# Kernel optimization log

Hardware: AMD Instinct MI355X
Metric: run time of the kernel (lower is better)

Reference implementation:

```python
import jax, jax.numpy as jnp
import numpy as np

S, D = 4096, 2048  # seq_len, embedding_space == qkv_dim


def setup_inputs() -> dict:
    key = jax.random.key(0)
    k1, k2, k3, k4, k5 = jax.random.split(key, 5)
    return {
        "input_embedding": jax.random.normal(k1, (S, D), dtype=jnp.float32),
        "query_embedding": jax.random.normal(k2, (S, D), dtype=jnp.float32),
        "Wq": jax.random.normal(k3, (D, D), dtype=jnp.float32) * 0.02,
        "Wk": jax.random.normal(k4, (D, D), dtype=jnp.float32) * 0.02,
        "Wv": jax.random.normal(k5, (D, D), dtype=jnp.float32) * 0.02,
        "include_mask": 0,  # False -> causal mask applied (module's inverted logic)
    }


def reference(input_embedding, query_embedding, Wq, Wk, Wv, include_mask):
    q = query_embedding @ Wq          # [S, D]
    k = input_embedding @ Wk          # [S, D]
    v = input_embedding @ Wv          # [S, D]
    scores = (q @ k.T) / 10.0         # [S, S]; module hardcodes /10, not sqrt(d)
    if not include_mask:
        # causal: -inf strictly above the diagonal (triu with offset 1)
        s = scores.shape[0]
        causal = jnp.tril(jnp.ones((s, s), dtype=bool))
        scores = jnp.where(causal, scores, -jnp.inf)
    probs = jax.nn.softmax(scores, axis=-1)
    return probs @ v                  # [S, D]
```

## Files before the change

### kernel.cpp

```cpp
#include <hip/hip_runtime.h>
#include <hip/hip_bf16.h>
#include <math.h>

typedef __bf16 bf16_t;
typedef __bf16 bf16x8 __attribute__((ext_vector_type(8)));
typedef float f32x4 __attribute__((ext_vector_type(4)));

enum { EP_BF16 = 0, EP_SCORES = 1, EP_F32 = 2 };

__device__ __forceinline__ void gload_lds16(const void* g, void* l) {
  __builtin_amdgcn_global_load_lds(
      (const __attribute__((address_space(1))) void*)g,
      (__attribute__((address_space(3))) void*)l, 16, 0, 0);
}

__device__ __forceinline__ int xcd_swz(int bid, int nwg) {
  const int q = nwg >> 3;
  return (bid & 7) * q + (bid >> 3);
}


template <int TM, bool STG>
__device__ __forceinline__ void do_tile(char* smem, int slot, int sslot, size_t stoff,
                                        const char* const* gbase, const int* lbase,
                                        const int* aoff, const int* boff,
                                        f32x4 (&acc)[TM][4]) {
  bf16x8 bfr[4], af[4];
  if constexpr (TM == 8) {
    if constexpr (STG) {
      gload_lds16(gbase[0] + stoff, smem + sslot + lbase[0]);
      gload_lds16(gbase[1] + stoff, smem + sslot + lbase[1]);
    }
#pragma unroll
    for (int n = 0; n < 4; ++n) bfr[n] = *(const bf16x8*)(smem + slot + boff[n]);
#pragma unroll
    for (int m = 0; m < 4; ++m) af[m] = *(const bf16x8*)(smem + slot + aoff[m]);
    __builtin_amdgcn_s_setprio(1);
#pragma unroll
    for (int m = 0; m < 4; ++m)
#pragma unroll
      for (int n = 0; n < 4; ++n)
        acc[m][n] = __builtin_amdgcn_mfma_f32_16x16x32_bf16(af[m], bfr[n], acc[m][n], 0, 0, 0);
    __builtin_amdgcn_s_setprio(0);
    if constexpr (STG) __builtin_amdgcn_s_barrier();
    if constexpr (STG) {
      gload_lds16(gbase[2] + stoff, smem + sslot + lbase[2]);
      gload_lds16(gbase[3] + stoff, smem + sslot + lbase[3]);
    }
#pragma unroll
    for (int m = 0; m < 4; ++m) af[m] = *(const bf16x8*)(smem + slot + aoff[4 + m]);
    __builtin_amdgcn_s_setprio(1);
#pragma unroll
    for (int m = 0; m < 4; ++m)
#pragma unroll
      for (int n = 0; n < 4; ++n)
        acc[4 + m][n] = __builtin_amdgcn_mfma_f32_16x16x32_bf16(af[m], bfr[n], acc[4 + m][n], 0, 0, 0);
    __builtin_amdgcn_s_setprio(0);
  } else {
    if constexpr (STG) {
      gload_lds16(gbase[0] + stoff, smem + sslot + lbase[0]);
      gload_lds16(gbase[1] + stoff, smem + sslot + lbase[1]);
      gload_lds16(gbase[2] + stoff, smem + sslot + lbase[2]);
    }
#pragma unroll
    for (int n = 0; n < 4; ++n) bfr[n] = *(const bf16x8*)(smem + slot + boff[n]);
#pragma unroll
    for (int m = 0; m < 4; ++m) af[m] = *(const bf16x8*)(smem + slot + aoff[m]);
    __builtin_amdgcn_s_setprio(1);
#pragma unroll
    for (int m = 0; m < 4; ++m)
#pragma unroll
      for (int n = 0; n < 4; ++n)
        acc[m][n] = __builtin_amdgcn_mfma_f32_16x16x32_bf16(af[m], bfr[n], acc[m][n], 0, 0, 0);
    __builtin_amdgcn_s_setprio(0);
  }
}

template <int TM, int EPI>
__device__ __forceinline__ void gemm_core(
    const bf16_t* __restrict__ A, const bf16_t* __restrict__ B,
    void* __restrict__ Cout, int M, int N, int K,
    int row0, int col0, bool causal, float scale, char* smem)
{
  constexpr int BM = TM * 32;
  constexpr int LPT_A = BM / 128;
  constexpr int LPT = LPT_A + 2;
  constexpr int ABYTES = BM * 64;
  constexpr int SLOT = (BM + 256) * 64;

  const int tid = threadIdx.x;
  const int w = tid >> 6, lane = tid & 63;
  const int wr = w >> 2, wc = w & 3;

  int Keff = K;
  if (EPI == EP_F32 && causal) Keff = min(K, row0 + BM);
  const int nt = Keff >> 5;

  const char* gbase[LPT];
  int lbase[LPT];
  {
    const int sd = (tid & 3) ^ ((tid >> 3) & 3);
    const int rrow = tid >> 2;
#pragma unroll
    for (int r = 0; r < LPT; ++r) {
      const bool isA = (r < LPT_A);
      const int rr = isA ? r : (r - LPT_A);
      const int R = rr * 128 + rrow;
      const int grow = (isA ? row0 : col0) + R;
      const bf16_t* op = isA ? A : B;
      gbase[r] = (const char*)(op + (size_t)grow * K) + sd * 16;
      lbase[r] = (isA ? 0 : ABYTES) + rr * 8192 + w * 1024;
    }
  }

  const int fl = lane & 15;
  const int arow_off = fl * 64 + (((lane >> 4) ^ ((fl >> 1) & 3)) * 16);
  int aoff[TM], boff[4];
#pragma unroll
  for (int m = 0; m < TM; ++m) aoff[m] = (wr * (TM * 16) + m * 16) * 64 + arow_off;
#pragma unroll
  for (int n = 0; n < 4; ++n) boff[n] = ABYTES + (wc * 64 + n * 16) * 64 + arow_off;

  f32x4 acc[TM][4] = {};

  const int npro = nt < 3 ? nt : 3;
  for (int t = 0; t < npro; ++t)
#pragma unroll
    for (int r = 0; r < LPT; ++r)
      gload_lds16(gbase[r] + (size_t)t * 64, smem + (t & 3) * SLOT + lbase[r]);

  const int nmain = nt - 3;
  for (int t = 0; t < nmain; ++t) {
    if constexpr (TM == 8) asm volatile("s_waitcnt vmcnt(8)" ::: "memory");
    else                   asm volatile("s_waitcnt vmcnt(6)" ::: "memory");
    __builtin_amdgcn_s_barrier();
    asm volatile("" ::: "memory");
    __builtin_amdgcn_sched_barrier(0);
    do_tile<TM, true>(smem, (t & 3) * SLOT, ((t + 3) & 3) * SLOT,
                      (size_t)(t + 3) * 64, gbase, lbase, aoff, boff, acc);
  }

  asm volatile("s_waitcnt vmcnt(0)" ::: "memory");
  __builtin_amdgcn_s_barrier();
  asm volatile("" ::: "memory");
  __builtin_amdgcn_sched_barrier(0);
  for (int t = nmain > 0 ? nmain : 0; t < nt; ++t)
    do_tile<TM, false>(smem, (t & 3) * SLOT, 0, 0, gbase, lbase, aoff, boff, acc);

  const int cr = (lane >> 4) * 4;
  const int cc = lane & 15;
#pragma unroll
  for (int m = 0; m < TM; ++m) {
#pragma unroll
    for (int n = 0; n < 4; ++n) {
#pragma unroll
      for (int i = 0; i < 4; ++i) {
        const int r = row0 + wr * (TM * 16) + m * 16 + cr + i;
        const int c = col0 + wc * 64 + n * 16 + cc;
        float v = acc[m][n][i];
        if (EPI == EP_BF16) {
          ((bf16_t*)Cout)[(size_t)r * N + c] = (bf16_t)v;
        } else if (EPI == EP_SCORES) {
          v *= scale;
          if (causal && c > r) v = -INFINITY;
          ((float*)Cout)[(size_t)r * N + c] = v;
        } else {
          ((float*)Cout)[(size_t)r * N + c] = v;
        }
      }
    }
  }
}

__launch_bounds__(512, 2)
__global__ void qk_k(const bf16_t* __restrict__ qe16, const bf16_t* __restrict__ ie16,
                     const bf16_t* __restrict__ WqT, const bf16_t* __restrict__ WkT,
                     bf16_t* __restrict__ q16, bf16_t* __restrict__ k16) {
  extern __shared__ __align__(16) char smem[];
  int wg = xcd_swz(blockIdx.x, gridDim.x);
  const bf16_t *A, *B; bf16_t* C;
  if (wg < 128) { A = qe16; B = WqT; C = q16; }
  else          { A = ie16; B = WkT; C = k16; wg -= 128; }
  const int row0 = (wg >> 3) * 256, col0 = (wg & 7) * 256;
  gemm_core<8, EP_BF16>(A, B, C, 4096, 2048, 2048, row0, col0, false, 1.f, smem);
}

__launch_bounds__(512, 2)
__global__ void vs_k(const bf16_t* __restrict__ WvT, const bf16_t* __restrict__ ie16,
                     const bf16_t* __restrict__ q16, const bf16_t* __restrict__ k16,
                     bf16_t* __restrict__ vT16, float* __restrict__ scores,
                     const int* __restrict__ maskflag) {
  extern __shared__ __align__(16) char smem[];
  int wg = xcd_swz(blockIdx.x, gridDim.x);
  if (wg < 128) {
    const int row0 = (wg >> 4) * 256, col0 = (wg & 15) * 256;
    gemm_core<8, EP_BF16>(WvT, ie16, vT16, 2048, 4096, 2048, row0, col0, false, 1.f, smem);
  } else {
    const int sid = wg - 128;
    const bool causal = maskflag[0] == 0;
    int r, c;
    if (causal) {
      if (sid >= 136) return;
      r = (int)((sqrtf(8.f * (float)sid + 1.f) - 1.f) * 0.5f);
      while ((r + 1) * (r + 2) / 2 <= sid) ++r;
      while (r * (r + 1) / 2 > sid) --r;
      c = sid - r * (r + 1) / 2;
    } else {
      r = sid >> 4; c = sid & 15;
    }
    gemm_core<8, EP_SCORES>(q16, k16, scores, 4096, 4096, 2048,
                            r * 256, c * 256, causal, 0.1f, smem);
  }
}

template <int TM, int EPI>
__launch_bounds__(512, 2)
__global__ void gemm_k(const bf16_t* __restrict__ A, const bf16_t* __restrict__ B,
                       void* __restrict__ C, int M, int N, int K,
                       const int* __restrict__ maskflag, float scale) {
  extern __shared__ __align__(16) char smem[];
  const bool causal = (maskflag != nullptr) && (maskflag[0] == 0);
  constexpr int BM = TM * 32;
  const int ntn = N >> 8;
  const int wg = xcd_swz(blockIdx.x, gridDim.x);
  const int row0 = (wg / ntn) * BM, col0 = (wg % ntn) * 256;
  gemm_core<TM, EPI>(A, B, C, M, N, K, row0, col0, causal, scale, smem);
}


__global__ void cvt_k(const float* __restrict__ qe, const float* __restrict__ ie,
                      bf16_t* __restrict__ qe16, bf16_t* __restrict__ ie16, long n) {
  const float* x = blockIdx.y ? ie : qe;
  bf16_t* y = blockIdx.y ? ie16 : qe16;
  long i = ((long)blockIdx.x * blockDim.x + threadIdx.x) * 8;
  const long stride = (long)gridDim.x * blockDim.x * 8;
  for (; i < n; i += stride) {
    const float4 a = *(const float4*)(x + i);
    const float4 b = *(const float4*)(x + i + 4);
    bf16x8 o;
    o[0] = (__bf16)a.x; o[1] = (__bf16)a.y; o[2] = (__bf16)a.z; o[3] = (__bf16)a.w;
    o[4] = (__bf16)b.x; o[5] = (__bf16)b.y; o[6] = (__bf16)b.z; o[7] = (__bf16)b.w;
    *(bf16x8*)(y + i) = o;
  }
}

__global__ void trans_k(const float* __restrict__ Wq, const float* __restrict__ Wk,
                        const float* __restrict__ Wv,
                        bf16_t* __restrict__ WqT, bf16_t* __restrict__ WkT,
                        bf16_t* __restrict__ WvT, int Dm) {
  const float* W = blockIdx.z == 0 ? Wq : (blockIdx.z == 1 ? Wk : Wv);
  bf16_t* WT = blockIdx.z == 0 ? WqT : (blockIdx.z == 1 ? WkT : WvT);
  __shared__ float tile[32][33];
  const int bx = blockIdx.x, by = blockIdx.y;
  const int tx = threadIdx.x & 31, ty = threadIdx.x >> 5;
#pragma unroll
  for (int r = ty; r < 32; r += 8)
    tile[r][tx] = W[(size_t)(by * 32 + r) * Dm + bx * 32 + tx];
  __syncthreads();
#pragma unroll
  for (int r = ty; r < 32; r += 8)
    WT[(size_t)(bx * 32 + r) * Dm + by * 32 + tx] = (bf16_t)tile[tx][r];
}

__global__ void softmax_rows(const float* __restrict__ Sc, bf16_t* __restrict__ P,
                             int n, const int* __restrict__ maskflag) {
  const int row = blockIdx.x;
  const int tid = threadIdx.x;
  const bool causal = maskflag[0] == 0;
  const int L = causal ? (row + 1) : n;
  const float* srow = Sc + (size_t)row * n;
  float v[16];
  float m = -INFINITY;
#pragma unroll
  for (int j = 0; j < 16; ++j) {
    const int idx = tid + j * 256;
    v[j] = (idx < L) ? srow[idx] : -INFINITY;
    m = fmaxf(m, v[j]);
  }
#pragma unroll
  for (int off = 32; off >= 1; off >>= 1) m = fmaxf(m, __shfl_xor(m, off));
  __shared__ float redm[4];
  __shared__ float reds[4];
  if ((tid & 63) == 0) redm[tid >> 6] = m;
  __syncthreads();
  m = fmaxf(fmaxf(redm[0], redm[1]), fmaxf(redm[2], redm[3]));
  float s = 0.f;
#pragma unroll
  for (int j = 0; j < 16; ++j) {
    v[j] = __expf(v[j] - m);
    s += v[j];
  }
#pragma unroll
  for (int off = 32; off >= 1; off >>= 1) s += __shfl_xor(s, off);
  if ((tid & 63) == 0) reds[tid >> 6] = s;
  __syncthreads();
  s = reds[0] + reds[1] + reds[2] + reds[3];
  const float inv = 1.f / s;
  bf16_t* prow = P + (size_t)row * n;
#pragma unroll
  for (int j = 0; j < 16; ++j) prow[tid + j * 256] = (bf16_t)(v[j] * inv);
}

extern "C" void kernel_launch(void* const* d_in, const int* in_sizes, int n_in,
                              void* d_out, int out_size, void* d_ws, size_t ws_size,
                              hipStream_t stream) {
  const float* ie = (const float*)d_in[0];
  const float* qe = (const float*)d_in[1];
  const float* Wq = (const float*)d_in[2];
  const float* Wk = (const float*)d_in[3];
  const float* Wv = (const float*)d_in[4];
  const int* mask = (const int*)d_in[5];
  float* out = (float*)d_out;

  const int S = 4096, D = 2048;
  char* ws = (char*)d_ws;
  const size_t MB = 1u << 20;
  bf16_t* q16  = (bf16_t*)(ws + 0 * MB);
  bf16_t* k16  = (bf16_t*)(ws + 16 * MB);
  bf16_t* vT16 = (bf16_t*)(ws + 32 * MB);
  bf16_t* ie16 = (bf16_t*)(ws + 48 * MB);
  bf16_t* WvT  = (bf16_t*)(ws + 64 * MB);
  bf16_t* qe16 = (bf16_t*)(ws + 72 * MB);
  bf16_t* WqT  = (bf16_t*)(ws + 88 * MB);
  bf16_t* WkT  = (bf16_t*)(ws + 96 * MB);
  float*  scores = (float*)(ws + 72 * MB);
  bf16_t* probs  = (bf16_t*)(ws + 0 * MB);

  hipFuncSetAttribute(reinterpret_cast<const void*>(&qk_k),
                      hipFuncAttributeMaxDynamicSharedMemorySize, 131072);
  hipFuncSetAttribute(reinterpret_cast<const void*>(&vs_k),
                      hipFuncAttributeMaxDynamicSharedMemorySize, 131072);
  hipFuncSetAttribute(reinterpret_cast<const void*>(&gemm_k<4, EP_F32>),
                      hipFuncAttributeMaxDynamicSharedMemorySize, 98304);

  cvt_k<<<dim3(1024, 2), 256, 0, stream>>>(qe, ie, qe16, ie16, (long)S * D);
  trans_k<<<dim3(D / 32, D / 32, 3), 256, 0, stream>>>(Wq, Wk, Wv, WqT, WkT, WvT, D);

  qk_k<<<256, 512, 131072, stream>>>(qe16, ie16, WqT, WkT, q16, k16);

  vs_k<<<384, 512, 131072, stream>>>(WvT, ie16, q16, k16, vT16, scores, mask);

  softmax_rows<<<S, 256, 0, stream>>>(scores, probs, S, mask);

  gemm_k<4, EP_F32><<<256, 512, 98304, stream>>>(probs, vT16, out, S, D, S, mask, 1.f);
}
```

Before: 294.8 us.

## Restructure GEMM tile pipeline with extra barriers and rebalance V/score grid

The MFMA tile loop is reordered so LDS fragment reads are issued before the global-to-LDS prefetch, and explicit barriers, lgkmcnt waits and vmcnt waits are placed around each MFMA phase, in a ping-pong style schedule. The combined V-projection/scores kernel now puts score tiles first with their own XCD swizzle, and computes V with 128-row tiles (TM=4) over 256 blocks instead of 128 blocks of 256 rows. This is meant to better overlap loads with MFMA work and to balance the causal score tiles against the V GEMM. In exchange it adds several workgroup barriers per k-step and launches more blocks, some of which exit immediately in the causal case.

```diff
diff --git a/kernel.cpp b/kernel.cpp
--- a/kernel.cpp
+++ b/kernel.cpp
@@ -7,6 +7,9 @@
 typedef float f32x4 __attribute__((ext_vector_type(4)));
 
 enum { EP_BF16 = 0, EP_SCORES = 1, EP_F32 = 2 };
+
+#define MEMFENCE asm volatile("" ::: "memory")
+#define BARRIER() do { MEMFENCE; __builtin_amdgcn_s_barrier(); MEMFENCE; } while (0)
 
 __device__ __forceinline__ void gload_lds16(const void* g, void* l) {
   __builtin_amdgcn_global_load_lds(
@@ -27,14 +30,17 @@
                                         f32x4 (&acc)[TM][4]) {
   bf16x8 bfr[4], af[4];
   if constexpr (TM == 8) {
+#pragma unroll
+    for (int n = 0; n < 4; ++n) bfr[n] = *(const bf16x8*)(smem + slot + boff[n]);
+#pragma unroll
+    for (int m = 0; m < 4; ++m) af[m] = *(const bf16x8*)(smem + slot + aoff[m]);
     if constexpr (STG) {
       gload_lds16(gbase[0] + stoff, smem + sslot + lbase[0]);
       gload_lds16(gbase[1] + stoff, smem + sslot + lbase[1]);
     }
-#pragma unroll
-    for (int n = 0; n < 4; ++n) bfr[n] = *(const bf16x8*)(smem + slot + boff[n]);
-#pragma unroll
-    for (int m = 0; m < 4; ++m) af[m] = *(const bf16x8*)(smem + slot + aoff[m]);
+    BARRIER();
+    asm volatile("s_waitcnt lgkmcnt(0)" ::: "memory");
+    __builtin_amdgcn_sched_barrier(0);
     __builtin_amdgcn_s_setprio(1);
 #pragma unroll
     for (int m = 0; m < 4; ++m)
@@ -42,13 +48,17 @@
       for (int n = 0; n < 4; ++n)
         acc[m][n] = __builtin_amdgcn_mfma_f32_16x16x32_bf16(af[m], bfr[n], acc[m][n], 0, 0, 0);
     __builtin_amdgcn_s_setprio(0);
-    if constexpr (STG) __builtin_amdgcn_s_barrier();
+    BARRIER();
+#pragma unroll
+    for (int m = 0; m < 4; ++m) af[m] = *(const bf16x8*)(smem + slot + aoff[4 + m]);
     if constexpr (STG) {
       gload_lds16(gbase[2] + stoff, smem + sslot + lbase[2]);
       gload_lds16(gbase[3] + stoff, smem + sslot + lbase[3]);
-    }
-#pragma unroll
-    for (int m = 0; m < 4; ++m) af[m] = *(const bf16x8*)(smem + slot + aoff[4 + m]);
+      asm volatile("s_waitcnt vmcnt(8)" ::: "memory");
+    }
+    BARRIER();
+    asm volatile("s_waitcnt lgkmcnt(0)" ::: "memory");
+    __builtin_amdgcn_sched_barrier(0);
     __builtin_amdgcn_s_setprio(1);
 #pragma unroll
     for (int m = 0; m < 4; ++m)
@@ -56,16 +66,21 @@
       for (int n = 0; n < 4; ++n)
         acc[4 + m][n] = __builtin_amdgcn_mfma_f32_16x16x32_bf16(af[m], bfr[n], acc[4 + m][n], 0, 0, 0);
     __builtin_amdgcn_s_setprio(0);
+    BARRIER();
   } else {
+#pragma unroll
+    for (int n = 0; n < 4; ++n) bfr[n] = *(const bf16x8*)(smem + slot + boff[n]);
+#pragma unroll
+    for (int m = 0; m < 4; ++m) af[m] = *(const bf16x8*)(smem + slot + aoff[m]);
     if constexpr (STG) {
       gload_lds16(gbase[0] + stoff, smem + sslot + lbase[0]);
       gload_lds16(gbase[1] + stoff, smem + sslot + lbase[1]);
       gload_lds16(gbase[2] + stoff, smem + sslot + lbase[2]);
-    }
-#pragma unroll
-    for (int n = 0; n < 4; ++n) bfr[n] = *(const bf16x8*)(smem + slot + boff[n]);
-#pragma unroll
-    for (int m = 0; m < 4; ++m) af[m] = *(const bf16x8*)(smem + slot + aoff[m]);
+      asm volatile("s_waitcnt vmcnt(6)" ::: "memory");
+    }
+    BARRIER();
+    asm volatile("s_waitcnt lgkmcnt(0)" ::: "memory");
+    __builtin_amdgcn_sched_barrier(0);
     __builtin_amdgcn_s_setprio(1);
 #pragma unroll
     for (int m = 0; m < 4; ++m)
@@ -73,6 +88,7 @@
       for (int n = 0; n < 4; ++n)
         acc[m][n] = __builtin_amdgcn_mfma_f32_16x16x32_bf16(af[m], bfr[n], acc[m][n], 0, 0, 0);
     __builtin_amdgcn_s_setprio(0);
+    BARRIER();
   }
 }
 
@@ -105,8 +121,7 @@
     for (int r = 0; r < LPT; ++r) {
       const bool isA = (r < LPT_A);
       const int rr = isA ? r : (r - LPT_A);
-      const int R = rr * 128 + rrow;
-      const int grow = (isA ? row0 : col0) + R;
+      const int grow = (isA ? row0 : col0) + rr * 128 + rrow;
       const bf16_t* op = isA ? A : B;
       gbase[r] = (const char*)(op + (size_t)grow * K) + sd * 16;
       lbase[r] = (isA ? 0 : ABYTES) + rr * 8192 + w * 1024;
@@ -130,20 +145,17 @@
       gload_lds16(gbase[r] + (size_t)t * 64, smem + (t & 3) * SLOT + lbase[r]);
 
   const int nmain = nt - 3;
-  for (int t = 0; t < nmain; ++t) {
+  if (nmain > 0) {
     if constexpr (TM == 8) asm volatile("s_waitcnt vmcnt(8)" ::: "memory");
     else                   asm volatile("s_waitcnt vmcnt(6)" ::: "memory");
-    __builtin_amdgcn_s_barrier();
-    asm volatile("" ::: "memory");
-    __builtin_amdgcn_sched_barrier(0);
-    do_tile<TM, true>(smem, (t & 3) * SLOT, ((t + 3) & 3) * SLOT,
-                      (size_t)(t + 3) * 64, gbase, lbase, aoff, boff, acc);
+    BARRIER();
+    for (int t = 0; t < nmain; ++t)
+      do_tile<TM, true>(smem, (t & 3) * SLOT, ((t + 3) & 3) * SLOT,
+                        (size_t)(t + 3) * 64, gbase, lbase, aoff, boff, acc);
   }
 
   asm volatile("s_waitcnt vmcnt(0)" ::: "memory");
-  __builtin_amdgcn_s_barrier();
-  asm volatile("" ::: "memory");
-  __builtin_amdgcn_sched_barrier(0);
+  BARRIER();
   for (int t = nmain > 0 ? nmain : 0; t < nt; ++t)
     do_tile<TM, false>(smem, (t & 3) * SLOT, 0, 0, gbase, lbase, aoff, boff, acc);
 
@@ -191,16 +203,13 @@
                      bf16_t* __restrict__ vT16, float* __restrict__ scores,
                      const int* __restrict__ maskflag) {
   extern __shared__ __align__(16) char smem[];
-  int wg = xcd_swz(blockIdx.x, gridDim.x);
-  if (wg < 128) {
-    const int row0 = (wg >> 4) * 256, col0 = (wg & 15) * 256;
-    gemm_core<8, EP_BF16>(WvT, ie16, vT16, 2048, 4096, 2048, row0, col0, false, 1.f, smem);
-  } else {
-    const int sid = wg - 128;
-    const bool causal = maskflag[0] == 0;
+  const bool causal = maskflag[0] == 0;
+  const int bid = blockIdx.x;
+  const int nsc = causal ? 136 : 256;
+  if (bid < nsc) {
+    const int sid = xcd_swz(bid, nsc);
     int r, c;
     if (causal) {
-      if (sid >= 136) return;
       r = (int)((sqrtf(8.f * (float)sid + 1.f) - 1.f) * 0.5f);
       while ((r + 1) * (r + 2) / 2 <= sid) ++r;
       while (r * (r + 1) / 2 > sid) --r;
@@ -210,6 +219,12 @@
     }
     gemm_core<8, EP_SCORES>(q16, k16, scores, 4096, 4096, 2048,
                             r * 256, c * 256, causal, 0.1f, smem);
+  } else {
+    const int vloc = bid - nsc;
+    if (vloc >= 256) return;
+    const int wg = xcd_swz(vloc, 256);
+    const int row0 = (wg >> 4) * 128, col0 = (wg & 15) * 256;
+    gemm_core<4, EP_BF16>(WvT, ie16, vT16, 2048, 4096, 2048, row0, col0, false, 1.f, smem);
   }
 }
 
@@ -338,7 +353,7 @@
 
   qk_k<<<256, 512, 131072, stream>>>(qe16, ie16, WqT, WkT, q16, k16);
 
-  vs_k<<<384, 512, 131072, stream>>>(WvT, ie16, q16, k16, vT16, scores, mask);
+  vs_k<<<512, 512, 131072, stream>>>(WvT, ie16, q16, k16, vT16, scores, mask);
 
   softmax_rows<<<S, 256, 0, stream>>>(scores, probs, S, mask);
 
```

Result: faster. 275.3 us (-6.6%).
